# Optimization experiments

Hardware: AMD Instinct MI355X
Metric: run time of the kernel (lower is better)

## Reference

```python
import jax, jax.numpy as jnp
import numpy as np

N, D_IN, D_H, D_O, N_CLS, E = 8192, 512, 256, 128, 8, 262144


def setup_inputs() -> dict:
    key = jax.random.key(0)
    ks = jax.random.split(key, 21)
    def unif(k, shape, fan):
        s = 1.0 / np.sqrt(fan)
        return jax.random.uniform(k, shape, jnp.float32, -s, s)
    return {
        "feats": jax.random.normal(ks[0], (N, D_IN), jnp.float32),
        "norm": jax.random.uniform(ks[1], (N, 1), jnp.float32),
        "tao_1_L": jax.random.normal(ks[2], (D_H, D_H), jnp.float32) * (1.0 / np.sqrt(D_H)),
        "tao_2_L": jax.random.normal(ks[3], (D_O, D_O), jnp.float32) * (1.0 / np.sqrt(D_O)),
        "tao_1_G": jax.random.normal(ks[4], (D_H, D_H), jnp.float32) * (1.0 / np.sqrt(D_H)),
        "tao_2_G": jax.random.normal(ks[5], (D_O, D_O), jnp.float32) * (1.0 / np.sqrt(D_O)),
        # dense PPMI matrix, scaled so row-sums are O(1)
        "PPMI": jax.random.uniform(ks[6], (N, N), jnp.float32) * (1.0 / N),
        # local-branch GCN params (reset_parameters: uniform(-1/sqrt(fan), +))
        "w1": unif(ks[7], (D_IN, D_H), D_H),
        "b1": unif(ks[8], (D_H,), D_IN),
        "w2": unif(ks[9], (D_H, D_O), D_O),
        "b2": unif(ks[10], (D_O,), D_H),
        # global (PPMI)-branch GCN params
        "w1g": unif(ks[11], (D_IN, D_H), D_H),
        "b1g": unif(ks[12], (D_H,), D_IN),
        "w2g": unif(ks[13], (D_H, D_O), D_O),
        "b2g": unif(ks[14], (D_O,), D_H),
        # attention and classifier params
        "W_a": unif(ks[15], (2 * D_O, 2), 2),
        "W_c": unif(ks[16], (D_O, N_CLS), N_CLS),
        "b_c": unif(ks[17], (N_CLS,), D_O),
        # graph edge list (src -> dst)
        "src": jax.random.randint(ks[18], (E,), 0, N),
        "dst": jax.random.randint(ks[19], (E,), 0, N),
    }


def _gcn_prop(h, src, dst, norm):
    # DGL update_all(gcn_msg, gcn_reduce): msg = h[src]*norm[src],
    # accum = segment_sum over dst, then scale by dst norm.
    msg = h[src] * norm[src]                               # [E, d]
    agg = jax.ops.segment_sum(msg, dst, num_segments=N)    # [N, d]
    return agg * norm


def reference(feats, norm, tao_1_L, tao_2_L, tao_1_G, tao_2_G, PPMI,
              w1, b1, w2, b2, w1g, b1g, w2g, b2g, W_a, W_c, b_c,
              src, dst):
    relu = jax.nn.relu
    # ---- local branch (edge-list GCN) ----
    h = feats @ (w1 @ tao_1_L)                             # [N, D_H]
    h = relu(_gcn_prop(h, src, dst, norm) + b1)
    h = h @ (w2 @ tao_2_L)                                 # [N, D_O]
    H_L = relu(_gcn_prop(h, src, dst, norm) + b2)
    # ---- global branch (dense PPMI propagation) ----
    h = PPMI @ (feats @ (w1g @ tao_1_G))
    h = relu(h + b1g)
    h = PPMI @ (h @ (w2g @ tao_2_G))
    H_G = relu(h + b2g)
    # ---- attention fusion ----
    attn = jax.nn.softmax(jnp.concatenate([H_L, H_G], axis=1) @ W_a, axis=1)  # [N, 2]
    Z = attn[:, :1] * H_L + attn[:, 1:] * H_G
    # ---- classifier ----
    return Z @ W_c + b_c
```

## Files before the change

### kernel.cpp

```cpp
#include <hip/hip_runtime.h>
#include <hip/hip_bf16.h>

#define NN 8192
#define DIN 512
#define DH 256
#define DO_ 128
#define NCLS 8
#define NE 262144

typedef __attribute__((ext_vector_type(8))) short bf16x8;
typedef __attribute__((ext_vector_type(4))) float f32x4;
typedef __attribute__((ext_vector_type(4))) unsigned short u16x4;
typedef __attribute__((ext_vector_type(8))) unsigned short u16x8;

__device__ __forceinline__ unsigned short f2bf(float x) {
    unsigned int u = __float_as_uint(x);
    return (unsigned short)((u + 0x7FFFu + ((u >> 16) & 1u)) >> 16);
}
__device__ __forceinline__ float bf2f(unsigned short h) {
    return __uint_as_float((unsigned int)h << 16);
}

#define GLDS(gp, lp) __builtin_amdgcn_global_load_lds( \
    (const __attribute__((address_space(1))) void*)(gp), \
    (__attribute__((address_space(3))) void*)(lp), 16, 0, 0)

__device__ __forceinline__ void cvt8_store(unsigned short* dst, float4 a, float4 b) {
    u16x8 o;
    o[0] = f2bf(a.x); o[1] = f2bf(a.y); o[2] = f2bf(a.z); o[3] = f2bf(a.w);
    o[4] = f2bf(b.x); o[5] = f2bf(b.y); o[6] = f2bf(b.z); o[7] = f2bf(b.w);
    *(u16x8*)dst = o;
}


__device__ void dev_gemm_split(int bx, int by,
                               const unsigned short* __restrict__ Ah, const unsigned short* __restrict__ Al,
                               const unsigned short* __restrict__ Bh, const unsigned short* __restrict__ Bl,
                               float* __restrict__ C, int M, int N, int K) {
    __shared__ unsigned short AsH[128 * 32];
    __shared__ unsigned short AsL[128 * 32];
    __shared__ unsigned short BsH[128 * 32];
    __shared__ unsigned short BsL[128 * 32];
    const int t = threadIdx.x;
    const int w = t >> 6;
    const int l = t & 63;
    const int wr = (w >> 1) * 64;
    const int wc = (w & 1) * 64;
    const long row0 = (long)bx * 128;
    const long col0 = (long)by * 128;
    const int nk = K >> 5;

    f32x4 acc[4][4];
#pragma unroll
    for (int mi = 0; mi < 4; ++mi)
#pragma unroll
        for (int ni = 0; ni < 4; ++ni) { f32x4 z = {0.f,0.f,0.f,0.f}; acc[mi][ni] = z; }

    const int srow = (w << 4) + (l >> 2);
    const int skk  = (l & 3) << 3;
    const long aoff = row0 * K + skk;
    const long boff = col0 * K + skk;
    unsigned short* AsHW = &AsH[w << 9];
    unsigned short* AsLW = &AsL[w << 9];
    unsigned short* BsHW = &BsH[w << 9];
    unsigned short* BsLW = &BsL[w << 9];

    for (int kt = 0; kt < nk; ++kt) {
        const long ko = (long)kt << 5;
        __syncthreads();
        GLDS(Ah + aoff + (long)srow * K + ko,        AsHW);
        GLDS(Ah + aoff + (long)(srow + 64) * K + ko, AsHW + 2048);
        GLDS(Al + aoff + (long)srow * K + ko,        AsLW);
        GLDS(Al + aoff + (long)(srow + 64) * K + ko, AsLW + 2048);
        GLDS(Bh + boff + (long)srow * K + ko,        BsHW);
        GLDS(Bh + boff + (long)(srow + 64) * K + ko, BsHW + 2048);
        GLDS(Bl + boff + (long)srow * K + ko,        BsLW);
        GLDS(Bl + boff + (long)(srow + 64) * K + ko, BsLW + 2048);
        __syncthreads();

        const int ro  = (l & 15);
        const int kof = (l >> 4) << 3;
        bf16x8 ah[4], al[4], bh[4], bl[4];
#pragma unroll
        for (int mi = 0; mi < 4; ++mi) {
            ah[mi] = *(const bf16x8*)&AsH[(wr + mi * 16 + ro) * 32 + kof];
            al[mi] = *(const bf16x8*)&AsL[(wr + mi * 16 + ro) * 32 + kof];
        }
#pragma unroll
        for (int ni = 0; ni < 4; ++ni) {
            bh[ni] = *(const bf16x8*)&BsH[(wc + ni * 16 + ro) * 32 + kof];
            bl[ni] = *(const bf16x8*)&BsL[(wc + ni * 16 + ro) * 32 + kof];
        }
#pragma unroll
        for (int mi = 0; mi < 4; ++mi)
#pragma unroll
            for (int ni = 0; ni < 4; ++ni) {
                acc[mi][ni] = __builtin_amdgcn_mfma_f32_16x16x32_bf16(ah[mi], bl[ni], acc[mi][ni], 0, 0, 0);
                acc[mi][ni] = __builtin_amdgcn_mfma_f32_16x16x32_bf16(al[mi], bh[ni], acc[mi][ni], 0, 0, 0);
                acc[mi][ni] = __builtin_amdgcn_mfma_f32_16x16x32_bf16(ah[mi], bh[ni], acc[mi][ni], 0, 0, 0);
            }
    }
#pragma unroll
    for (int mi = 0; mi < 4; ++mi)
#pragma unroll
        for (int ni = 0; ni < 4; ++ni) {
            const long col = col0 + wc + ni * 16 + (l & 15);
            const long rbase = row0 + wr + mi * 16 + ((l >> 4) << 2);
            f32x4 v = acc[mi][ni];
#pragma unroll
            for (int j = 0; j < 4; ++j) C[(rbase + j) * N + col] = v[j];
        }
}

__device__ void dev_gemm_b1(int bx, int by,
                            const unsigned short* __restrict__ A, const unsigned short* __restrict__ B,
                            unsigned short* __restrict__ C, int M, int N, int K) {
    __shared__ unsigned short As1[128 * 32];
    __shared__ unsigned short Bs1[128 * 32];
    const int t = threadIdx.x;
    const int w = t >> 6;
    const int l = t & 63;
    const int wr = (w >> 1) * 64;
    const int wc = (w & 1) * 64;
    const long row0 = (long)bx * 128;
    const long col0 = (long)by * 128;
    const int nk = K >> 5;

    f32x4 acc[4][4];
#pragma unroll
    for (int mi = 0; mi < 4; ++mi)
#pragma unroll
        for (int ni = 0; ni < 4; ++ni) { f32x4 z = {0.f,0.f,0.f,0.f}; acc[mi][ni] = z; }

    const int srow = (w << 4) + (l >> 2);
    const int skk  = (l & 3) << 3;
    const unsigned short* Abase = A + row0 * K + skk;
    const unsigned short* Bbase = B + col0 * K + skk;
    unsigned short* AsW = &As1[w << 9];
    unsigned short* BsW = &Bs1[w << 9];

    for (int kt = 0; kt < nk; ++kt) {
        const long ko = (long)kt << 5;
        __syncthreads();
        GLDS(Abase + (long)srow * K + ko,        AsW);
        GLDS(Abase + (long)(srow + 64) * K + ko, AsW + 2048);
        GLDS(Bbase + (long)srow * K + ko,        BsW);
        GLDS(Bbase + (long)(srow + 64) * K + ko, BsW + 2048);
        __syncthreads();

        const int ro  = (l & 15);
        const int kof = (l >> 4) << 3;
        bf16x8 a[4], b[4];
#pragma unroll
        for (int mi = 0; mi < 4; ++mi)
            a[mi] = *(const bf16x8*)&As1[(wr + mi * 16 + ro) * 32 + kof];
#pragma unroll
        for (int ni = 0; ni < 4; ++ni)
            b[ni] = *(const bf16x8*)&Bs1[(wc + ni * 16 + ro) * 32 + kof];
#pragma unroll
        for (int mi = 0; mi < 4; ++mi)
#pragma unroll
            for (int ni = 0; ni < 4; ++ni)
                acc[mi][ni] = __builtin_amdgcn_mfma_f32_16x16x32_bf16(a[mi], b[ni], acc[mi][ni], 0, 0, 0);
    }
#pragma unroll
    for (int mi = 0; mi < 4; ++mi)
#pragma unroll
        for (int ni = 0; ni < 4; ++ni) {
            const long col = col0 + wc + ni * 16 + (l & 15);
            const long rbase = row0 + wr + mi * 16 + ((l >> 4) << 2);
            f32x4 v = acc[mi][ni];
            u16x4 o;
            o.x = f2bf(v[0]); o.y = f2bf(v[1]); o.z = f2bf(v[2]); o.w = f2bf(v[3]);
            *(u16x4*)(C + col * M + rbase) = o;
        }
}

__device__ void dev_ppmi1(int bx, int z, const float* __restrict__ A,
                          const unsigned short* __restrict__ B, unsigned short* __restrict__ C) {
    __shared__ unsigned short AsP[128 * 32];
    __shared__ unsigned short BsP[256 * 32];
    const int t = threadIdx.x;
    const int w = t >> 6;
    const int l = t & 63;
    const int wr = (w >> 2) * 64;
    const int wc = (w & 3) * 64;
    const long row0 = (long)bx * 128;
    const long kbeg = (long)z * (NN / 8);
    const int nk = (NN / 8) >> 5;
    const int K = NN;

    f32x4 acc[4][4];
#pragma unroll
    for (int mi = 0; mi < 4; ++mi)
#pragma unroll
        for (int ni = 0; ni < 4; ++ni) { f32x4 zz = {0.f,0.f,0.f,0.f}; acc[mi][ni] = zz; }

    const int ar = t >> 2;
    const int akq = (t & 3) << 3;
    const float* Abase = A + (row0 + ar) * K + kbeg + akq;
    unsigned short* AsW = &AsP[ar * 32 + akq];
    const int srow = (w << 4) + (l >> 2);
    const int skk  = (l & 3) << 3;
    const unsigned short* Bbase = B + (long)srow * K + kbeg + skk;
    unsigned short* BsW = &BsP[(w << 4) * 32];

    for (int kt = 0; kt < nk; ++kt) {
        const long ko = (long)kt << 5;
        __syncthreads();
        float4 fa0 = *(const float4*)(Abase + ko);
        float4 fa1 = *(const float4*)(Abase + ko + 4);
        GLDS(Bbase + ko,                 BsW);
        GLDS(Bbase + (long)128 * K + ko, BsW + 128 * 32);
        cvt8_store(AsW, fa0, fa1);
        __syncthreads();

        const int ro  = (l & 15);
        const int kof = (l >> 4) << 3;
        bf16x8 a[4], b[4];
#pragma unroll
        for (int mi = 0; mi < 4; ++mi)
            a[mi] = *(const bf16x8*)&AsP[(wr + mi * 16 + ro) * 32 + kof];
#pragma unroll
        for (int ni = 0; ni < 4; ++ni)
            b[ni] = *(const bf16x8*)&BsP[(wc + ni * 16 + ro) * 32 + kof];
#pragma unroll
        for (int mi = 0; mi < 4; ++mi)
#pragma unroll
            for (int ni = 0; ni < 4; ++ni)
                acc[mi][ni] = __builtin_amdgcn_mfma_f32_16x16x32_bf16(a[mi], b[ni], acc[mi][ni], 0, 0, 0);
    }

    unsigned short* Cp = C + (long)z * NN * DH;
#pragma unroll
    for (int mi = 0; mi < 4; ++mi)
#pragma unroll
        for (int ni = 0; ni < 4; ++ni) {
            const long col = wc + ni * 16 + (l & 15);
            const long rbase = row0 + wr + mi * 16 + ((l >> 4) << 2);
            f32x4 v = acc[mi][ni];
#pragma unroll
            for (int j = 0; j < 4; ++j) Cp[(rbase + j) * DH + col] = f2bf(v[j]);
        }
}

__device__ void dev_ppmi2(int bx, int z, const float* __restrict__ A,
                          const unsigned short* __restrict__ B, unsigned short* __restrict__ C) {
    __shared__ unsigned short AsQ[128 * 32];
    __shared__ unsigned short BsQ[128 * 32];
    const int t = threadIdx.x;
    const int w = t >> 6;
    const int l = t & 63;
    const int wr = (w >> 1) * 64;
    const int wc = (w & 1) * 64;
    const long row0 = (long)bx * 128;
    const long kbeg = (long)z * (NN / 8);
    const int nk = (NN / 8) >> 5;
    const int K = NN;

    f32x4 acc[4][4];
#pragma unroll
    for (int mi = 0; mi < 4; ++mi)
#pragma unroll
        for (int ni = 0; ni < 4; ++ni) { f32x4 zz = {0.f,0.f,0.f,0.f}; acc[mi][ni] = zz; }

    const int ar = t >> 1;
    const int akh = (t & 1) << 4;
    const float* Abase = A + (row0 + ar) * K + kbeg + akh;
    unsigned short* AsW = &AsQ[ar * 32 + akh];
    const int srow = (w << 4) + (l >> 2);
    const int skk  = (l & 3) << 3;
    const unsigned short* Bbase = B + (long)srow * K + kbeg + skk;
    unsigned short* BsW = &BsQ[w << 9];

    for (int kt = 0; kt < nk; ++kt) {
        const long ko = (long)kt << 5;
        __syncthreads();
        float4 fa0 = *(const float4*)(Abase + ko);
        float4 fa1 = *(const float4*)(Abase + ko + 4);
        float4 fa2 = *(const float4*)(Abase + ko + 8);
        float4 fa3 = *(const float4*)(Abase + ko + 12);
        GLDS(Bbase + ko,                BsW);
        GLDS(Bbase + (long)64 * K + ko, BsW + 2048);
        cvt8_store(AsW,     fa0, fa1);
        cvt8_store(AsW + 8, fa2, fa3);
        __syncthreads();

        const int ro  = (l & 15);
        const int kof = (l >> 4) << 3;
        bf16x8 a[4], b[4];
#pragma unroll
        for (int mi = 0; mi < 4; ++mi)
            a[mi] = *(const bf16x8*)&AsQ[(wr + mi * 16 + ro) * 32 + kof];
#pragma unroll
        for (int ni = 0; ni < 4; ++ni)
            b[ni] = *(const bf16x8*)&BsQ[(wc + ni * 16 + ro) * 32 + kof];
#pragma unroll
        for (int mi = 0; mi < 4; ++mi)
#pragma unroll
            for (int ni = 0; ni < 4; ++ni)
                acc[mi][ni] = __builtin_amdgcn_mfma_f32_16x16x32_bf16(a[mi], b[ni], acc[mi][ni], 0, 0, 0);
    }

    unsigned short* Cp = C + (long)z * NN * DO_;
#pragma unroll
    for (int mi = 0; mi < 4; ++mi)
#pragma unroll
        for (int ni = 0; ni < 4; ++ni) {
            const long col = wc + ni * 16 + (l & 15);
            const long rbase = row0 + wr + mi * 16 + ((l >> 4) << 2);
            f32x4 v = acc[mi][ni];
#pragma unroll
            for (int j = 0; j < 4; ++j) Cp[(rbase + j) * DO_ + col] = f2bf(v[j]);
        }
}

__device__ void dev_g256(int row, const float* __restrict__ h,
                         const int* __restrict__ rs, const int* __restrict__ csrc,
                         const float* __restrict__ norm, const float* __restrict__ bias,
                         unsigned short* __restrict__ outh, unsigned short* __restrict__ outl) {
    __shared__ int   sh_s[256];
    __shared__ float sh_ns[256];
    __shared__ float shred[4 * 256];
    const int tid = threadIdx.x, wv = tid >> 6, l = tid & 63;
    const int beg = rs[row], end = rs[row + 1];
    float4 acc = make_float4(0.f, 0.f, 0.f, 0.f);
    for (int base = beg; base < end; base += 256) {
        __syncthreads();
        if (base + tid < end) {
            int s = csrc[base + tid];
            sh_s[tid] = s;
            sh_ns[tid] = norm[s];
        }
        __syncthreads();
        int cnt = min(256, end - base);
        for (int j = wv; j < cnt; j += 4) {
            int s = sh_s[j];
            float ns = sh_ns[j];
            float4 hv = *(const float4*)&h[((long)s << 8) + (l << 2)];
            acc.x += hv.x * ns; acc.y += hv.y * ns; acc.z += hv.z * ns; acc.w += hv.w * ns;
        }
    }
    __syncthreads();
    *(float4*)&shred[wv * 256 + (l << 2)] = acc;
    __syncthreads();
    float val = shred[tid] + shred[256 + tid] + shred[512 + tid] + shred[768 + tid];
    float r = fmaxf(val * norm[row] + bias[tid], 0.f);
    unsigned short hb = f2bf(r);
    outh[((long)row << 8) + tid] = hb;
    outl[((long)row << 8) + tid] = f2bf(r - bf2f(hb));
}

__device__ void dev_g128(int row, const float* __restrict__ h,
                         const int* __restrict__ rs, const int* __restrict__ csrc,
                         const float* __restrict__ norm, const float* __restrict__ bias,
                         float* __restrict__ out) {
    __shared__ int   sh_s2[256];
    __shared__ float sh_ns2[256];
    __shared__ float shred2[4 * 128];
    const int tid = threadIdx.x, wv = tid >> 6, l = tid & 63;
    const int beg = rs[row], end = rs[row + 1];
    float2 acc = make_float2(0.f, 0.f);
    for (int base = beg; base < end; base += 256) {
        __syncthreads();
        if (base + tid < end) {
            int s = csrc[base + tid];
            sh_s2[tid] = s;
            sh_ns2[tid] = norm[s];
        }
        __syncthreads();
        int cnt = min(256, end - base);
        for (int j = wv; j < cnt; j += 4) {
            int s = sh_s2[j];
            float ns = sh_ns2[j];
            float2 hv = *(const float2*)&h[((long)s << 7) + (l << 1)];
            acc.x += hv.x * ns; acc.y += hv.y * ns;
        }
    }
    __syncthreads();
    *(float2*)&shred2[wv * 128 + (l << 1)] = acc;
    __syncthreads();
    if (tid < 128) {
        float val = shred2[tid] + shred2[128 + tid] + shred2[256 + tid] + shred2[384 + tid];
        float r = fmaxf(val * norm[row] + bias[tid], 0.f);
        out[((long)row << 7) + tid] = r;
    }
}

__device__ void dev_c1(int idx, const unsigned short* __restrict__ part,
                       unsigned short* __restrict__ out, const float* __restrict__ bias) {
    int n4 = DH >> 2;
    if (idx >= NN * n4) return;
    int m = idx / n4, c = idx % n4;
    float4 s = make_float4(0.f, 0.f, 0.f, 0.f);
    for (int z = 0; z < 8; ++z) {
        u16x4 p = *(const u16x4*)&part[((long)z * NN + m) * DH + (c << 2)];
        s.x += bf2f(p.x); s.y += bf2f(p.y); s.z += bf2f(p.z); s.w += bf2f(p.w);
    }
    float4 b = *(const float4*)&bias[c << 2];
    u16x4 o;
    o.x = f2bf(fmaxf(s.x + b.x, 0.f));
    o.y = f2bf(fmaxf(s.y + b.y, 0.f));
    o.z = f2bf(fmaxf(s.z + b.z, 0.f));
    o.w = f2bf(fmaxf(s.w + b.w, 0.f));
    *(u16x4*)&out[(long)m * DH + (c << 2)] = o;
}

__device__ void dev_eff_split(int idx, const float* __restrict__ w, const float* __restrict__ tao,
                              unsigned short* __restrict__ th, unsigned short* __restrict__ tl,
                              int I, int K0, int J) {
    if (idx >= I * J) return;
    int j = idx % J, i = idx / J;
    float s = 0.f;
    for (int k = 0; k < K0; ++k) s += w[i * K0 + k] * tao[k * J + j];
    unsigned short h = f2bf(s);
    th[j * I + i] = h;
    tl[j * I + i] = f2bf(s - bf2f(h));
}
__device__ void dev_eff_hi(int idx, const float* __restrict__ w, const float* __restrict__ tao,
                           unsigned short* __restrict__ th, int I, int K0, int J) {
    if (idx >= I * J) return;
    int j = idx % J, i = idx / J;
    float s = 0.f;
    for (int k = 0; k < K0; ++k) s += w[i * K0 + k] * tao[k * J + j];
    th[j * I + i] = f2bf(s);
}

__device__ void dev_scan256(const int* __restrict__ deg, int* __restrict__ rs, int* __restrict__ cur) {
    __shared__ int sums[256];
    int t = threadIdx.x;
    int loc[32];
    int s = 0;
#pragma unroll
    for (int j = 0; j < 32; ++j) { loc[j] = deg[t * 32 + j]; s += loc[j]; }
    sums[t] = s;
    __syncthreads();
    for (int off = 1; off < 256; off <<= 1) {
        int v = (t >= off) ? sums[t - off] : 0;
        __syncthreads();
        sums[t] += v;
        __syncthreads();
    }
    int base = (t > 0) ? sums[t - 1] : 0;
#pragma unroll
    for (int j = 0; j < 32; ++j) {
        rs[t * 32 + j] = base;
        cur[t * 32 + j] = base;
        base += loc[j];
    }
    if (t == 255) rs[NN] = base;
}


__global__ __launch_bounds__(256) void k_s1(
    const int* __restrict__ dst, int* __restrict__ deg,
    const float* __restrict__ feats, unsigned short* __restrict__ fh, unsigned short* __restrict__ fl,
    const float* w1, const float* t1, unsigned short* e1h, unsigned short* e1l,
    const float* w2, const float* t2, unsigned short* e2h, unsigned short* e2l,
    const float* w3, const float* t3, unsigned short* e3h,
    const float* w4, const float* t4, unsigned short* e4h) {
    int b = blockIdx.x;
    if (b < 1024) {
        int e = b * 256 + threadIdx.x;
        atomicAdd(&deg[dst[e]], 1);
    } else if (b < 5120) {
        int i = (b - 1024) * 256 + threadIdx.x;
        float4 v = ((const float4*)feats)[i];
        u16x4 oh, ol;
        oh.x = f2bf(v.x); ol.x = f2bf(v.x - bf2f(oh.x));
        oh.y = f2bf(v.y); ol.y = f2bf(v.y - bf2f(oh.y));
        oh.z = f2bf(v.z); ol.z = f2bf(v.z - bf2f(oh.z));
        oh.w = f2bf(v.w); ol.w = f2bf(v.w - bf2f(oh.w));
        ((u16x4*)fh)[i] = oh;
        ((u16x4*)fl)[i] = ol;
    } else if (b < 5632) {
        dev_eff_split((b - 5120) * 256 + threadIdx.x, w1, t1, e1h, e1l, DIN, DH, DH);
    } else if (b < 5760) {
        dev_eff_split((b - 5632) * 256 + threadIdx.x, w2, t2, e2h, e2l, DH, DO_, DO_);
    } else if (b < 6272) {
        dev_eff_hi((b - 5760) * 256 + threadIdx.x, w3, t3, e3h, DIN, DH, DH);
    } else {
        dev_eff_hi((b - 6272) * 256 + threadIdx.x, w4, t4, e4h, DH, DO_, DO_);
    }
}

__global__ __launch_bounds__(256) void k_s2(
    const unsigned short* fh, const unsigned short* fl,
    const unsigned short* w1lh, const unsigned short* w1ll, float* h0,
    const unsigned short* w1gh, unsigned short* g0t,
    const int* deg, int* rs, int* cur) {
    int b = blockIdx.x;
    if (b < 128)      dev_gemm_split(b & 63, b >> 6, fh, fl, w1lh, w1ll, h0, NN, DH, DIN);
    else if (b < 256) dev_gemm_b1((b - 128) & 63, (b - 128) >> 6, fh, w1gh, g0t, NN, DH, DIN);
    else              dev_scan256(deg, rs, cur);
}

__global__ __launch_bounds__(512) void k_s3(
    const float* __restrict__ PPMI, const unsigned short* g0t, unsigned short* part1,
    const int* __restrict__ src, const int* __restrict__ dst, int* cur, int* csrc) {
    int b = blockIdx.x;
    if (b < 512) {
        dev_ppmi1(b & 63, b >> 6, PPMI, g0t, part1);
    } else {
        int e = (b - 512) * 512 + threadIdx.x;
        int pos = atomicAdd(&cur[dst[e]], 1);
        csrc[pos] = src[e];
    }
}

__global__ __launch_bounds__(256) void k_s4(
    const float* h0, const int* rs, const int* csrc, const float* norm, const float* b1,
    unsigned short* h1h, unsigned short* h1l,
    const unsigned short* part1, unsigned short* g2, const float* b1g) {
    int b = blockIdx.x;
    if (b < 8192) dev_g256(b, h0, rs, csrc, norm, b1, h1h, h1l);
    else          dev_c1((b - 8192) * 256 + threadIdx.x, part1, g2, b1g);
}

__global__ __launch_bounds__(256) void k_s5(
    const unsigned short* h1h, const unsigned short* h1l,
    const unsigned short* w2lh, const unsigned short* w2ll, float* h2,
    const unsigned short* g2, const unsigned short* w2gh, unsigned short* g3t) {
    int b = blockIdx.x;
    if (b < 64) dev_gemm_split(b, 0, h1h, h1l, w2lh, w2ll, h2, NN, DO_, DH);
    else        dev_gemm_b1(b - 64, 0, g2, w2gh, g3t, NN, DO_, DH);
}

__global__ __launch_bounds__(256) void k_s6(
    const float* __restrict__ PPMI, const unsigned short* g3t, unsigned short* part2,
    const float* h2, const int* rs, const int* csrc, const float* norm, const float* b2,
    float* HL) {
    int b = blockIdx.x;
    if (b < 512) dev_ppmi2(b & 63, b >> 6, PPMI, g3t, part2);
    else         dev_g128(b - 512, h2, rs, csrc, norm, b2, HL);
}

__global__ __launch_bounds__(256) void k_comb2(const unsigned short* __restrict__ part,
                                               float* __restrict__ out, const float* __restrict__ bias) {
    int idx = blockIdx.x * blockDim.x + threadIdx.x;
    int n4 = DO_ >> 2;
    if (idx >= NN * n4) return;
    int m = idx / n4, c = idx % n4;
    float4 s = make_float4(0.f, 0.f, 0.f, 0.f);
    for (int z = 0; z < 8; ++z) {
        u16x4 p = *(const u16x4*)&part[((long)z * NN + m) * DO_ + (c << 2)];
        s.x += bf2f(p.x); s.y += bf2f(p.y); s.z += bf2f(p.z); s.w += bf2f(p.w);
    }
    float4 b = *(const float4*)&bias[c << 2];
    s.x = fmaxf(s.x + b.x, 0.f);
    s.y = fmaxf(s.y + b.y, 0.f);
    s.z = fmaxf(s.z + b.z, 0.f);
    s.w = fmaxf(s.w + b.w, 0.f);
    *(float4*)(out + (long)m * DO_ + (c << 2)) = s;
}

__global__ __launch_bounds__(256) void k_attn(
    const float* __restrict__ HL, const float* __restrict__ HG,
    const float* __restrict__ Wa, const float* __restrict__ Wc,
    const float* __restrict__ bc, float* __restrict__ out) {
    int wv = threadIdx.x >> 6, l = threadIdx.x & 63;
    int row = blockIdx.x * 4 + wv;
    float2 hl = *(const float2*)&HL[(long)row * DO_ + l * 2];
    float2 hg = *(const float2*)&HG[(long)row * DO_ + l * 2];
    float4 wa0 = *(const float4*)&Wa[(2 * l) * 2];
    float4 wa1 = *(const float4*)&Wa[(DO_ + 2 * l) * 2];
    float p0 = hl.x * wa0.x + hl.y * wa0.z + hg.x * wa1.x + hg.y * wa1.z;
    float p1 = hl.x * wa0.y + hl.y * wa0.w + hg.x * wa1.y + hg.y * wa1.w;
#pragma unroll
    for (int off = 32; off >= 1; off >>= 1) {
        p0 += __shfl_xor(p0, off);
        p1 += __shfl_xor(p1, off);
    }
    float mx = fmaxf(p0, p1);
    float e0 = __expf(p0 - mx), e1 = __expf(p1 - mx);
    float inv = 1.f / (e0 + e1);
    float a0 = e0 * inv, a1 = e1 * inv;
    float z0 = a0 * hl.x + a1 * hg.x;
    float z1 = a0 * hl.y + a1 * hg.y;
    float4 wcA0 = *(const float4*)&Wc[(2 * l) * NCLS];
    float4 wcA1 = *(const float4*)&Wc[(2 * l) * NCLS + 4];
    float4 wcB0 = *(const float4*)&Wc[(2 * l + 1) * NCLS];
    float4 wcB1 = *(const float4*)&Wc[(2 * l + 1) * NCLS + 4];
    float q0 = z0 * wcA0.x + z1 * wcB0.x;
    float q1 = z0 * wcA0.y + z1 * wcB0.y;
    float q2 = z0 * wcA0.z + z1 * wcB0.z;
    float q3 = z0 * wcA0.w + z1 * wcB0.w;
    float q4 = z0 * wcA1.x + z1 * wcB1.x;
    float q5 = z0 * wcA1.y + z1 * wcB1.y;
    float q6 = z0 * wcA1.z + z1 * wcB1.z;
    float q7 = z0 * wcA1.w + z1 * wcB1.w;
#pragma unroll
    for (int off = 32; off >= 1; off >>= 1) {
        q0 += __shfl_xor(q0, off); q1 += __shfl_xor(q1, off);
        q2 += __shfl_xor(q2, off); q3 += __shfl_xor(q3, off);
        q4 += __shfl_xor(q4, off); q5 += __shfl_xor(q5, off);
        q6 += __shfl_xor(q6, off); q7 += __shfl_xor(q7, off);
    }
    if (l == 0) {
        float* o = &out[(long)row * NCLS];
        o[0] = q0 + bc[0]; o[1] = q1 + bc[1]; o[2] = q2 + bc[2]; o[3] = q3 + bc[3];
        o[4] = q4 + bc[4]; o[5] = q5 + bc[5]; o[6] = q6 + bc[6]; o[7] = q7 + bc[7];
    }
}

extern "C" void kernel_launch(void* const* d_in, const int* in_sizes, int n_in,
                              void* d_out, int out_size, void* d_ws, size_t ws_size,
                              hipStream_t stream) {
    (void)in_sizes; (void)n_in; (void)out_size; (void)ws_size;
    const float* feats = (const float*)d_in[0];
    const float* norm  = (const float*)d_in[1];
    const float* tao1L = (const float*)d_in[2];
    const float* tao2L = (const float*)d_in[3];
    const float* tao1G = (const float*)d_in[4];
    const float* tao2G = (const float*)d_in[5];
    const float* PPMI  = (const float*)d_in[6];
    const float* w1  = (const float*)d_in[7];
    const float* b1  = (const float*)d_in[8];
    const float* w2  = (const float*)d_in[9];
    const float* b2  = (const float*)d_in[10];
    const float* w1g = (const float*)d_in[11];
    const float* b1g = (const float*)d_in[12];
    const float* w2g = (const float*)d_in[13];
    const float* b2g = (const float*)d_in[14];
    const float* Wa  = (const float*)d_in[15];
    const float* Wc  = (const float*)d_in[16];
    const float* bc  = (const float*)d_in[17];
    const int* src = (const int*)d_in[18];
    const int* dst = (const int*)d_in[19];

    char* ws = (char*)d_ws;
    size_t off = 0;
    auto alloc = [&](size_t b) { void* p = (void*)(ws + off); off += (b + 255) & ~(size_t)255; return p; };
    unsigned short* fh = (unsigned short*)alloc((size_t)NN * DIN * 2);
    unsigned short* fl = (unsigned short*)alloc((size_t)NN * DIN * 2);
    unsigned short* w1lh = (unsigned short*)alloc((size_t)DH * DIN * 2);
    unsigned short* w1ll = (unsigned short*)alloc((size_t)DH * DIN * 2);
    unsigned short* w2lh = (unsigned short*)alloc((size_t)DO_ * DH * 2);
    unsigned short* w2ll = (unsigned short*)alloc((size_t)DO_ * DH * 2);
    unsigned short* w1gh = (unsigned short*)alloc((size_t)DH * DIN * 2);
    unsigned short* w2gh = (unsigned short*)alloc((size_t)DO_ * DH * 2);
    unsigned short* g0t = (unsigned short*)alloc((size_t)DH * NN * 2);
    unsigned short* g2  = (unsigned short*)alloc((size_t)NN * DH * 2);
    unsigned short* g3t = (unsigned short*)alloc((size_t)DO_ * NN * 2);
    unsigned short* h1h = (unsigned short*)alloc((size_t)NN * DH * 2);
    unsigned short* h1l = (unsigned short*)alloc((size_t)NN * DH * 2);
    float* h0 = (float*)alloc((size_t)NN * DH * 4);
    float* h2 = (float*)alloc((size_t)NN * DO_ * 4);
    float* HL = (float*)alloc((size_t)NN * DO_ * 4);
    float* HG = (float*)alloc((size_t)NN * DO_ * 4);
    unsigned short* part1 = (unsigned short*)alloc((size_t)8 * NN * DH * 2);
    unsigned short* part2 = (unsigned short*)alloc((size_t)8 * NN * DO_ * 2);
    int* deg  = (int*)alloc((size_t)NN * 4);
    int* rs   = (int*)alloc((size_t)(NN + 1) * 4);
    int* cur  = (int*)alloc((size_t)NN * 4);
    int* csrc = (int*)alloc((size_t)NE * 4);

    hipMemsetAsync(deg, 0, (size_t)NN * 4, stream);

    k_s1<<<dim3(6400), dim3(256), 0, stream>>>(
        dst, deg, feats, fh, fl,
        w1,  tao1L, w1lh, w1ll,
        w2,  tao2L, w2lh, w2ll,
        w1g, tao1G, w1gh,
        w2g, tao2G, w2gh);

    k_s2<<<dim3(257), dim3(256), 0, stream>>>(fh, fl, w1lh, w1ll, h0, w1gh, g0t, deg, rs, cur);

    k_s3<<<dim3(1024), dim3(512), 0, stream>>>(PPMI, g0t, part1, src, dst, cur, csrc);

    k_s4<<<dim3(10240), dim3(256), 0, stream>>>(h0, rs, csrc, norm, b1, h1h, h1l, part1, g2, b1g);

    k_s5<<<dim3(128), dim3(256), 0, stream>>>(h1h, h1l, w2lh, w2ll, h2, g2, w2gh, g3t);

    k_s6<<<dim3(8704), dim3(256), 0, stream>>>(PPMI, g3t, part2, h2, rs, csrc, norm, b2, HL);

    k_comb2<<<dim3(1024), dim3(256), 0, stream>>>(part2, HG, b2g);
    k_attn<<<dim3(2048), dim3(256), 0, stream>>>(HL, HG, Wa, Wc, bc, (float*)d_out);
}
```

Before: 348.7 us.

## Fuse feature bf16 split into first GEMMs and merge partial-sum combine into attention

```diff
diff --git a/kernel.cpp b/kernel.cpp
--- a/kernel.cpp
+++ b/kernel.cpp
@@ -31,12 +31,25 @@
     o[4] = f2bf(b.x); o[5] = f2bf(b.y); o[6] = f2bf(b.z); o[7] = f2bf(b.w);
     *(u16x8*)dst = o;
 }
-
-
-__device__ void dev_gemm_split(int bx, int by,
-                               const unsigned short* __restrict__ Ah, const unsigned short* __restrict__ Al,
-                               const unsigned short* __restrict__ Bh, const unsigned short* __restrict__ Bl,
-                               float* __restrict__ C, int M, int N, int K) {
+__device__ __forceinline__ void cvt8_split_store(unsigned short* dH, unsigned short* dL, float4 a, float4 b) {
+    u16x8 oh, ol;
+    unsigned short h;
+    h = f2bf(a.x); oh[0] = h; ol[0] = f2bf(a.x - bf2f(h));
+    h = f2bf(a.y); oh[1] = h; ol[1] = f2bf(a.y - bf2f(h));
+    h = f2bf(a.z); oh[2] = h; ol[2] = f2bf(a.z - bf2f(h));
+    h = f2bf(a.w); oh[3] = h; ol[3] = f2bf(a.w - bf2f(h));
+    h = f2bf(b.x); oh[4] = h; ol[4] = f2bf(b.x - bf2f(h));
+    h = f2bf(b.y); oh[5] = h; ol[5] = f2bf(b.y - bf2f(h));
+    h = f2bf(b.z); oh[6] = h; ol[6] = f2bf(b.z - bf2f(h));
+    h = f2bf(b.w); oh[7] = h; ol[7] = f2bf(b.w - bf2f(h));
+    *(u16x8*)dH = oh;
+    *(u16x8*)dL = ol;
+}
+
+
+__device__ void dev_ls1(int bx, int by, const float* __restrict__ A,
+                        const unsigned short* __restrict__ Bh, const unsigned short* __restrict__ Bl,
+                        float* __restrict__ C) {
     __shared__ unsigned short AsH[128 * 32];
     __shared__ unsigned short AsL[128 * 32];
     __shared__ unsigned short BsH[128 * 32];
@@ -48,6 +61,90 @@
     const int wc = (w & 1) * 64;
     const long row0 = (long)bx * 128;
     const long col0 = (long)by * 128;
+    const int K = DIN;
+    const int nk = DIN >> 5;
+
+    f32x4 acc[4][4];
+#pragma unroll
+    for (int mi = 0; mi < 4; ++mi)
+#pragma unroll
+        for (int ni = 0; ni < 4; ++ni) { f32x4 z = {0.f,0.f,0.f,0.f}; acc[mi][ni] = z; }
+
+    const int ar = t >> 1;
+    const int akh = (t & 1) << 4;
+    const float* Abase = A + (row0 + ar) * K + akh;
+    const int aoff = ar * 32 + akh;
+    const int srow = (w << 4) + (l >> 2);
+    const int skk  = (l & 3) << 3;
+    const unsigned short* BhB = Bh + (col0 + srow) * K + skk;
+    const unsigned short* BlB = Bl + (col0 + srow) * K + skk;
+    unsigned short* BsHW = &BsH[w << 9];
+    unsigned short* BsLW = &BsL[w << 9];
+
+    for (int kt = 0; kt < nk; ++kt) {
+        const long ko = (long)kt << 5;
+        __syncthreads();
+        float4 fa0 = *(const float4*)(Abase + ko);
+        float4 fa1 = *(const float4*)(Abase + ko + 4);
+        float4 fa2 = *(const float4*)(Abase + ko + 8);
+        float4 fa3 = *(const float4*)(Abase + ko + 12);
+        GLDS(BhB + ko,                BsHW);
+        GLDS(BhB + (long)64 * K + ko, BsHW + 2048);
+        GLDS(BlB + ko,                BsLW);
+        GLDS(BlB + (long)64 * K + ko, BsLW + 2048);
+        cvt8_split_store(&AsH[aoff],     &AsL[aoff],     fa0, fa1);
+        cvt8_split_store(&AsH[aoff + 8], &AsL[aoff + 8], fa2, fa3);
+        __syncthreads();
+
+        const int ro  = (l & 15);
+        const int kof = (l >> 4) << 3;
+        bf16x8 ah[4], al[4], bh[4], bl[4];
+#pragma unroll
+        for (int mi = 0; mi < 4; ++mi) {
+            ah[mi] = *(const bf16x8*)&AsH[(wr + mi * 16 + ro) * 32 + kof];
+            al[mi] = *(const bf16x8*)&AsL[(wr + mi * 16 + ro) * 32 + kof];
+        }
+#pragma unroll
+        for (int ni = 0; ni < 4; ++ni) {
+            bh[ni] = *(const bf16x8*)&BsH[(wc + ni * 16 + ro) * 32 + kof];
+            bl[ni] = *(const bf16x8*)&BsL[(wc + ni * 16 + ro) * 32 + kof];
+        }
+#pragma unroll
+        for (int mi = 0; mi < 4; ++mi)
+#pragma unroll
+            for (int ni = 0; ni < 4; ++ni) {
+                acc[mi][ni] = __builtin_amdgcn_mfma_f32_16x16x32_bf16(ah[mi], bl[ni], acc[mi][ni], 0, 0, 0);
+                acc[mi][ni] = __builtin_amdgcn_mfma_f32_16x16x32_bf16(al[mi], bh[ni], acc[mi][ni], 0, 0, 0);
+                acc[mi][ni] = __builtin_amdgcn_mfma_f32_16x16x32_bf16(ah[mi], bh[ni], acc[mi][ni], 0, 0, 0);
+            }
+    }
+#pragma unroll
+    for (int mi = 0; mi < 4; ++mi)
+#pragma unroll
+        for (int ni = 0; ni < 4; ++ni) {
+            const long col = col0 + wc + ni * 16 + (l & 15);
+            const long rbase = row0 + wr + mi * 16 + ((l >> 4) << 2);
+            f32x4 v = acc[mi][ni];
+#pragma unroll
+            for (int j = 0; j < 4; ++j) C[(rbase + j) * DH + col] = v[j];
+        }
+}
+
+__device__ void dev_gemm_split(int bx, int by,
+                               const unsigned short* __restrict__ Ah, const unsigned short* __restrict__ Al,
+                               const unsigned short* __restrict__ Bh, const unsigned short* __restrict__ Bl,
+                               float* __restrict__ C, int M, int N, int K) {
+    __shared__ unsigned short AsH2[128 * 32];
+    __shared__ unsigned short AsL2[128 * 32];
+    __shared__ unsigned short BsH2[128 * 32];
+    __shared__ unsigned short BsL2[128 * 32];
+    const int t = threadIdx.x;
+    const int w = t >> 6;
+    const int l = t & 63;
+    const int wr = (w >> 1) * 64;
+    const int wc = (w & 1) * 64;
+    const long row0 = (long)bx * 128;
+    const long col0 = (long)by * 128;
     const int nk = K >> 5;
 
     f32x4 acc[4][4];
@@ -60,10 +157,10 @@
     const int skk  = (l & 3) << 3;
     const long aoff = row0 * K + skk;
     const long boff = col0 * K + skk;
-    unsigned short* AsHW = &AsH[w << 9];
-    unsigned short* AsLW = &AsL[w << 9];
-    unsigned short* BsHW = &BsH[w << 9];
-    unsigned short* BsLW = &BsL[w << 9];
+    unsigned short* AsHW = &AsH2[w << 9];
+    unsigned short* AsLW = &AsL2[w << 9];
+    unsigned short* BsHW = &BsH2[w << 9];
+    unsigned short* BsLW = &BsL2[w << 9];
 
     for (int kt = 0; kt < nk; ++kt) {
         const long ko = (long)kt << 5;
@@ -83,13 +180,13 @@
         bf16x8 ah[4], al[4], bh[4], bl[4];
 #pragma unroll
         for (int mi = 0; mi < 4; ++mi) {
-            ah[mi] = *(const bf16x8*)&AsH[(wr + mi * 16 + ro) * 32 + kof];
-            al[mi] = *(const bf16x8*)&AsL[(wr + mi * 16 + ro) * 32 + kof];
+            ah[mi] = *(const bf16x8*)&AsH2[(wr + mi * 16 + ro) * 32 + kof];
+            al[mi] = *(const bf16x8*)&AsL2[(wr + mi * 16 + ro) * 32 + kof];
         }
 #pragma unroll
         for (int ni = 0; ni < 4; ++ni) {
-            bh[ni] = *(const bf16x8*)&BsH[(wc + ni * 16 + ro) * 32 + kof];
-            bl[ni] = *(const bf16x8*)&BsL[(wc + ni * 16 + ro) * 32 + kof];
+            bh[ni] = *(const bf16x8*)&BsH2[(wc + ni * 16 + ro) * 32 + kof];
+            bl[ni] = *(const bf16x8*)&BsL2[(wc + ni * 16 + ro) * 32 + kof];
         }
 #pragma unroll
         for (int mi = 0; mi < 4; ++mi)
@@ -109,6 +206,76 @@
             f32x4 v = acc[mi][ni];
 #pragma unroll
             for (int j = 0; j < 4; ++j) C[(rbase + j) * N + col] = v[j];
+        }
+}
+
+__device__ void dev_gb1(int bx, int by, const float* __restrict__ A,
+                        const unsigned short* __restrict__ B, unsigned short* __restrict__ C) {
+    __shared__ unsigned short AsG[128 * 32];
+    __shared__ unsigned short BsG[128 * 32];
+    const int t = threadIdx.x;
+    const int w = t >> 6;
+    const int l = t & 63;
+    const int wr = (w >> 1) * 64;
+    const int wc = (w & 1) * 64;
+    const long row0 = (long)bx * 128;
+    const long col0 = (long)by * 128;
+    const int K = DIN;
+    const int nk = DIN >> 5;
+
+    f32x4 acc[4][4];
+#pragma unroll
+    for (int mi = 0; mi < 4; ++mi)
+#pragma unroll
+        for (int ni = 0; ni < 4; ++ni) { f32x4 z = {0.f,0.f,0.f,0.f}; acc[mi][ni] = z; }
+
+    const int ar = t >> 1;
+    const int akh = (t & 1) << 4;
+    const float* Abase = A + (row0 + ar) * K + akh;
+    const int aoff = ar * 32 + akh;
+    const int srow = (w << 4) + (l >> 2);
+    const int skk  = (l & 3) << 3;
+    const unsigned short* Bbase = B + (col0 + srow) * K + skk;
+    unsigned short* BsW = &BsG[w << 9];
+
+    for (int kt = 0; kt < nk; ++kt) {
+        const long ko = (long)kt << 5;
+        __syncthreads();
+        float4 fa0 = *(const float4*)(Abase + ko);
+        float4 fa1 = *(const float4*)(Abase + ko + 4);
+        float4 fa2 = *(const float4*)(Abase + ko + 8);
+        float4 fa3 = *(const float4*)(Abase + ko + 12);
+        GLDS(Bbase + ko,                BsW);
+        GLDS(Bbase + (long)64 * K + ko, BsW + 2048);
+        cvt8_store(&AsG[aoff],     fa0, fa1);
+        cvt8_store(&AsG[aoff + 8], fa2, fa3);
+        __syncthreads();
+
+        const int ro  = (l & 15);
+        const int kof = (l >> 4) << 3;
+        bf16x8 a[4], b[4];
+#pragma unroll
+        for (int mi = 0; mi < 4; ++mi)
+            a[mi] = *(const bf16x8*)&AsG[(wr + mi * 16 + ro) * 32 + kof];
+#pragma unroll
+        for (int ni = 0; ni < 4; ++ni)
+            b[ni] = *(const bf16x8*)&BsG[(wc + ni * 16 + ro) * 32 + kof];
+#pragma unroll
+        for (int mi = 0; mi < 4; ++mi)
+#pragma unroll
+            for (int ni = 0; ni < 4; ++ni)
+                acc[mi][ni] = __builtin_amdgcn_mfma_f32_16x16x32_bf16(a[mi], b[ni], acc[mi][ni], 0, 0, 0);
+    }
+#pragma unroll
+    for (int mi = 0; mi < 4; ++mi)
+#pragma unroll
+        for (int ni = 0; ni < 4; ++ni) {
+            const long col = col0 + wc + ni * 16 + (l & 15);
+            const long rbase = row0 + wr + mi * 16 + ((l >> 4) << 2);
+            f32x4 v = acc[mi][ni];
+            u16x4 o;
+            o.x = f2bf(v[0]); o.y = f2bf(v[1]); o.z = f2bf(v[2]); o.w = f2bf(v[3]);
+            *(u16x4*)(C + col * NN + rbase) = o;
         }
 }
 
@@ -454,7 +621,6 @@
 
 __global__ __launch_bounds__(256) void k_s1(
     const int* __restrict__ dst, int* __restrict__ deg,
-    const float* __restrict__ feats, unsigned short* __restrict__ fh, unsigned short* __restrict__ fl,
     const float* w1, const float* t1, unsigned short* e1h, unsigned short* e1l,
     const float* w2, const float* t2, unsigned short* e2h, unsigned short* e2l,
     const float* w3, const float* t3, unsigned short* e3h,
@@ -463,35 +629,25 @@
     if (b < 1024) {
         int e = b * 256 + threadIdx.x;
         atomicAdd(&deg[dst[e]], 1);
-    } else if (b < 5120) {
-        int i = (b - 1024) * 256 + threadIdx.x;
-        float4 v = ((const float4*)feats)[i];
-        u16x4 oh, ol;
-        oh.x = f2bf(v.x); ol.x = f2bf(v.x - bf2f(oh.x));
-        oh.y = f2bf(v.y); ol.y = f2bf(v.y - bf2f(oh.y));
-        oh.z = f2bf(v.z); ol.z = f2bf(v.z - bf2f(oh.z));
-        oh.w = f2bf(v.w); ol.w = f2bf(v.w - bf2f(oh.w));
-        ((u16x4*)fh)[i] = oh;
-        ((u16x4*)fl)[i] = ol;
-    } else if (b < 5632) {
-        dev_eff_split((b - 5120) * 256 + threadIdx.x, w1, t1, e1h, e1l, DIN, DH, DH);
-    } else if (b < 5760) {
-        dev_eff_split((b - 5632) * 256 + threadIdx.x, w2, t2, e2h, e2l, DH, DO_, DO_);
-    } else if (b < 6272) {
-        dev_eff_hi((b - 5760) * 256 + threadIdx.x, w3, t3, e3h, DIN, DH, DH);
+    } else if (b < 1536) {
+        dev_eff_split((b - 1024) * 256 + threadIdx.x, w1, t1, e1h, e1l, DIN, DH, DH);
+    } else if (b < 1664) {
+        dev_eff_split((b - 1536) * 256 + threadIdx.x, w2, t2, e2h, e2l, DH, DO_, DO_);
+    } else if (b < 2176) {
+        dev_eff_hi((b - 1664) * 256 + threadIdx.x, w3, t3, e3h, DIN, DH, DH);
     } else {
-        dev_eff_hi((b - 6272) * 256 + threadIdx.x, w4, t4, e4h, DH, DO_, DO_);
+        dev_eff_hi((b - 2176) * 256 + threadIdx.x, w4, t4, e4h, DH, DO_, DO_);
     }
 }
 
 __global__ __launch_bounds__(256) void k_s2(
-    const unsigned short* fh, const unsigned short* fl,
+    const float* __restrict__ feats,
     const unsigned short* w1lh, const unsigned short* w1ll, float* h0,
     const unsigned short* w1gh, unsigned short* g0t,
     const int* deg, int* rs, int* cur) {
     int b = blockIdx.x;
-    if (b < 128)      dev_gemm_split(b & 63, b >> 6, fh, fl, w1lh, w1ll, h0, NN, DH, DIN);
-    else if (b < 256) dev_gemm_b1((b - 128) & 63, (b - 128) >> 6, fh, w1gh, g0t, NN, DH, DIN);
+    if (b < 128)      dev_ls1(b & 63, b >> 6, feats, w1lh, w1ll, h0);
+    else if (b < 256) dev_gb1((b - 128) & 63, (b - 128) >> 6, feats, w1gh, g0t);
     else              dev_scan256(deg, rs, cur);
 }
 
@@ -535,33 +691,25 @@
     else         dev_g128(b - 512, h2, rs, csrc, norm, b2, HL);
 }
 
-__global__ __launch_bounds__(256) void k_comb2(const unsigned short* __restrict__ part,
-                                               float* __restrict__ out, const float* __restrict__ bias) {
-    int idx = blockIdx.x * blockDim.x + threadIdx.x;
-    int n4 = DO_ >> 2;
-    if (idx >= NN * n4) return;
-    int m = idx / n4, c = idx % n4;
-    float4 s = make_float4(0.f, 0.f, 0.f, 0.f);
-    for (int z = 0; z < 8; ++z) {
-        u16x4 p = *(const u16x4*)&part[((long)z * NN + m) * DO_ + (c << 2)];
-        s.x += bf2f(p.x); s.y += bf2f(p.y); s.z += bf2f(p.z); s.w += bf2f(p.w);
-    }
-    float4 b = *(const float4*)&bias[c << 2];
-    s.x = fmaxf(s.x + b.x, 0.f);
-    s.y = fmaxf(s.y + b.y, 0.f);
-    s.z = fmaxf(s.z + b.z, 0.f);
-    s.w = fmaxf(s.w + b.w, 0.f);
-    *(float4*)(out + (long)m * DO_ + (c << 2)) = s;
-}
-
-__global__ __launch_bounds__(256) void k_attn(
-    const float* __restrict__ HL, const float* __restrict__ HG,
+__global__ __launch_bounds__(256) void k_s7(
+    const float* __restrict__ HL, const unsigned short* __restrict__ part2,
+    const float* __restrict__ b2g,
     const float* __restrict__ Wa, const float* __restrict__ Wc,
     const float* __restrict__ bc, float* __restrict__ out) {
     int wv = threadIdx.x >> 6, l = threadIdx.x & 63;
     int row = blockIdx.x * 4 + wv;
+    float2 hg = make_float2(0.f, 0.f);
+#pragma unroll
+    for (int z = 0; z < 8; ++z) {
+        unsigned int u = *(const unsigned int*)&part2[((long)z * NN + row) * DO_ + 2 * l];
+        hg.x += bf2f((unsigned short)(u & 0xffffu));
+        hg.y += bf2f((unsigned short)(u >> 16));
+    }
+    float2 bg = *(const float2*)&b2g[2 * l];
+    hg.x = fmaxf(hg.x + bg.x, 0.f);
+    hg.y = fmaxf(hg.y + bg.y, 0.f);
+
     float2 hl = *(const float2*)&HL[(long)row * DO_ + l * 2];
-    float2 hg = *(const float2*)&HG[(long)row * DO_ + l * 2];
     float4 wa0 = *(const float4*)&Wa[(2 * l) * 2];
     float4 wa1 = *(const float4*)&Wa[(DO_ + 2 * l) * 2];
     float p0 = hl.x * wa0.x + hl.y * wa0.z + hg.x * wa1.x + hg.y * wa1.z;
@@ -631,8 +779,6 @@
     char* ws = (char*)d_ws;
     size_t off = 0;
     auto alloc = [&](size_t b) { void* p = (void*)(ws + off); off += (b + 255) & ~(size_t)255; return p; };
-    unsigned short* fh = (unsigned short*)alloc((size_t)NN * DIN * 2);
-    unsigned short* fl = (unsigned short*)alloc((size_t)NN * DIN * 2);
     unsigned short* w1lh = (unsigned short*)alloc((size_t)DH * DIN * 2);
     unsigned short* w1ll = (unsigned short*)alloc((size_t)DH * DIN * 2);
     unsigned short* w2lh = (unsigned short*)alloc((size_t)DO_ * DH * 2);
@@ -647,7 +793,6 @@
     float* h0 = (float*)alloc((size_t)NN * DH * 4);
     float* h2 = (float*)alloc((size_t)NN * DO_ * 4);
     float* HL = (float*)alloc((size_t)NN * DO_ * 4);
-    float* HG = (float*)alloc((size_t)NN * DO_ * 4);
     unsigned short* part1 = (unsigned short*)alloc((size_t)8 * NN * DH * 2);
     unsigned short* part2 = (unsigned short*)alloc((size_t)8 * NN * DO_ * 2);
     int* deg  = (int*)alloc((size_t)NN * 4);
@@ -657,14 +802,14 @@
 
     hipMemsetAsync(deg, 0, (size_t)NN * 4, stream);
 
-    k_s1<<<dim3(6400), dim3(256), 0, stream>>>(
-        dst, deg, feats, fh, fl,
+    k_s1<<<dim3(2304), dim3(256), 0, stream>>>(
+        dst, deg,
         w1,  tao1L, w1lh, w1ll,
         w2,  tao2L, w2lh, w2ll,
         w1g, tao1G, w1gh,
         w2g, tao2G, w2gh);
 
-    k_s2<<<dim3(257), dim3(256), 0, stream>>>(fh, fl, w1lh, w1ll, h0, w1gh, g0t, deg, rs, cur);
+    k_s2<<<dim3(257), dim3(256), 0, stream>>>(feats, w1lh, w1ll, h0, w1gh, g0t, deg, rs, cur);
 
     k_s3<<<dim3(1024), dim3(512), 0, stream>>>(PPMI, g0t, part1, src, dst, cur, csrc);
 
@@ -674,6 +819,5 @@
 
     k_s6<<<dim3(8704), dim3(256), 0, stream>>>(PPMI, g3t, part2, h2, rs, csrc, norm, b2, HL);
 
-    k_comb2<<<dim3(1024), dim3(256), 0, stream>>>(part2, HG, b2g);
-    k_attn<<<dim3(2048), dim3(256), 0, stream>>>(HL, HG, Wa, Wc, bc, (float*)d_out);
-}
+    k_s7<<<dim3(2048), dim3(256), 0, stream>>>(HL, part2, b2g, Wa, Wc, bc, (float*)d_out);
+}
```

Result: faster. 331.9 us (-4.8%).
